# Performance work log

Measured on AMD Instinct MI355X. Metric: run time of the kernel, lower is better.

Reference implementation:

```python
import jax, jax.numpy as jnp
import numpy as np

N_OCTAVES = 32
N_SAMPLES = 32768
SAMPLERATE = 22050
MIN_HZ = 20
MAX_HZ = 3000
BASE_RESONANCE = 0.01


def setup_inputs() -> dict:
    key = jax.random.key(0)
    k1, k2, k3 = jax.random.split(key, 3)
    B, E = 4, 16
    return {
        "f0": jax.random.uniform(k1, (B, E, 1), dtype=jnp.float32),
        "decay_coefficients": jax.random.normal(k2, (B, E, 1), dtype=jnp.float32),
        "freq_spacing": jax.random.uniform(k3, (B, E, 1), dtype=jnp.float32),
    }


def reference(f0, decay_coefficients, freq_spacing):
    B, E, _ = f0.shape
    min_freq = MIN_HZ / (SAMPLERATE // 2)
    max_freq = MAX_HZ / (SAMPLERATE // 2)
    freq_range = max_freq - min_freq

    f0 = jnp.abs(f0)  # (B, E, 1)

    # exponential_decay: note the forward applies sigmoid BEFORE calling
    # exponential_decay, which applies sigmoid again -> double sigmoid.
    dv = jax.nn.sigmoid(jax.nn.sigmoid(decay_coefficients))  # (B, E, 1)
    resonance_factor = (1.0 - BASE_RESONANCE) * 0.99
    d = BASE_RESONANCE + dv * resonance_factor  # (B, E, 1)
    log_d = jnp.broadcast_to(jnp.log(d + 1e-12), (B, E, N_OCTAVES))
    # interpolate(size=n_frames) with in==out size is the identity, so skip it.
    exp_decays = jnp.exp(jnp.cumsum(log_d, axis=-1))  # (B, E, O)

    f0 = (min_freq + f0 * freq_range) * np.pi  # (B, E, 1)
    factors = jnp.cumsum(jnp.broadcast_to(freq_spacing, (B, E, N_OCTAVES)), axis=-1)
    f0s = f0 * factors  # (B, E, O)
    f0s = f0s * (f0s < 1).astype(f0s.dtype)  # mask partials above Nyquist

    # cumsum of a constant per-sample frequency == freq * (sample_index + 1)
    t = jnp.arange(1, N_SAMPLES + 1, dtype=f0s.dtype)  # (S,)
    phase = f0s[..., None] * t  # (B, E, O, S)
    osc = jnp.sin(phase) * exp_decays[..., None]  # (B, E, O, S)

    osc = jnp.sum(osc, axis=2)  # (B, E, S)
    mx = jnp.max(jnp.abs(osc), axis=-1, keepdims=True)
    return osc / (mx + 1e-8)
```

## Files before the change

kernel.cpp:

```cpp
#include <hip/hip_runtime.h>
#include <math.h>

#define N_OCT  32
#define N_SMP  32768
#define N_PAIR 64
#define BPP    32

__global__ __launch_bounds__(256) void f0res_osc(
    const float* __restrict__ f0_in,
    const float* __restrict__ dec_in,
    const float* __restrict__ fs_in,
    float* __restrict__ out,
    float* __restrict__ bmax)
{
    __shared__ __align__(16) float sw[N_OCT];
    __shared__ __align__(16) float sa[N_OCT];

    const int pair = blockIdx.x >> 5;
    const int blk  = blockIdx.x & (BPP - 1);
    const int tid  = threadIdx.x;

    if (tid < N_OCT) {
        const float minf   = (float)(20.0 / 11025.0);
        const float frange = (float)(3000.0 / 11025.0 - 20.0 / 11025.0);
        const float pif    = 3.14159265358979323846f;
        const float INV2PI = 0.15915494309189535f;

        float f0 = fabsf(f0_in[pair]);
        float fs = fs_in[pair];
        float x  = dec_in[pair];

        float s1 = 1.0f / (1.0f + expf(-x));
        float s2 = 1.0f / (1.0f + expf(-s1));
        float d  = 0.01f + s2 * (float)(0.99 * 0.99);
        float ld = logf(d + 1e-12f);
        float f0p = (minf + f0 * frange) * pif;

        float fac = 0.0f, acl = 0.0f, myfac = 0.0f, myacl = 0.0f;
#pragma unroll
        for (int o = 0; o < N_OCT; ++o) {
            fac += fs;
            acl += ld;
            if (o == tid) { myfac = fac; myacl = acl; }
        }
        float f0s = f0p * myfac;
        sw[tid] = (f0s < 1.0f) ? f0s * INV2PI : 0.0f;
        sa[tid] = expf(myacl);
    }
    __syncthreads();

    float4 wv[8], av[8];
    const float4* w4 = (const float4*)sw;
    const float4* a4 = (const float4*)sa;
#pragma unroll
    for (int i = 0; i < 8; ++i) { wv[i] = w4[i]; av[i] = a4[i]; }

    const int   s0 = (blk << 10) + tid;
    const float t0 = (float)(s0 + 1);
    const float t1 = (float)(s0 + 257);
    const float t2 = (float)(s0 + 513);
    const float t3 = (float)(s0 + 769);

    float acc0 = 0.0f, acc1 = 0.0f, acc2 = 0.0f, acc3 = 0.0f;
#pragma unroll
    for (int i = 0; i < 8; ++i) {
        const float wr[4] = { wv[i].x, wv[i].y, wv[i].z, wv[i].w };
        const float ar[4] = { av[i].x, av[i].y, av[i].z, av[i].w };
#pragma unroll
        for (int j = 0; j < 4; ++j) {
            float w = wr[j], a = ar[j];
            acc0 = fmaf(a, __builtin_amdgcn_sinf(__builtin_amdgcn_fractf(w * t0)), acc0);
            acc1 = fmaf(a, __builtin_amdgcn_sinf(__builtin_amdgcn_fractf(w * t1)), acc1);
            acc2 = fmaf(a, __builtin_amdgcn_sinf(__builtin_amdgcn_fractf(w * t2)), acc2);
            acc3 = fmaf(a, __builtin_amdgcn_sinf(__builtin_amdgcn_fractf(w * t3)), acc3);
        }
    }

    float* op = out + pair * N_SMP + s0;
    op[0]   = acc0;
    op[256] = acc1;
    op[512] = acc2;
    op[768] = acc3;

    float av_ = fmaxf(fmaxf(fabsf(acc0), fabsf(acc1)),
                      fmaxf(fabsf(acc2), fabsf(acc3)));
#pragma unroll
    for (int m = 32; m >= 1; m >>= 1)
        av_ = fmaxf(av_, __shfl_xor(av_, m, 64));
    __shared__ float wm[4];
    if ((tid & 63) == 0) wm[tid >> 6] = av_;
    __syncthreads();
    if (tid == 0)
        bmax[pair * BPP + blk] = fmaxf(fmaxf(wm[0], wm[1]), fmaxf(wm[2], wm[3]));
}

__global__ __launch_bounds__(256) void f0res_norm(
    float* __restrict__ out, const float* __restrict__ bmax)
{
    const int pair = blockIdx.x >> 5;
    const int tid  = threadIdx.x;

    float v = (tid < BPP) ? bmax[pair * BPP + tid] : 0.0f;
#pragma unroll
    for (int m = 16; m >= 1; m >>= 1)
        v = fmaxf(v, __shfl_xor(v, m, 64));
    v = __shfl(v, 0, 64);
    __shared__ float smx;
    if (tid == 0) smx = v;
    __syncthreads();
    const float inv = 1.0f / (smx + 1e-8f);

    const int idx = ((blockIdx.x & 31) << 8) + tid;
    float4* o4 = (float4*)(out + pair * N_SMP);
    float4 val = o4[idx];
    val.x *= inv; val.y *= inv; val.z *= inv; val.w *= inv;
    o4[idx] = val;
}

extern "C" void kernel_launch(void* const* d_in, const int* in_sizes, int n_in,
                              void* d_out, int out_size, void* d_ws, size_t ws_size,
                              hipStream_t stream) {
    const float* f0  = (const float*)d_in[0];
    const float* dec = (const float*)d_in[1];
    const float* fs  = (const float*)d_in[2];
    float* out = (float*)d_out;

    float* bmax = (float*)d_ws;

    f0res_osc <<<N_PAIR * BPP, 256, 0, stream>>>(f0, dec, fs, out, bmax);
    f0res_norm<<<N_PAIR * 32,  256, 0, stream>>>(out, bmax);
}
```

Baseline: 74.18 us.

## Replace per-sample sin with angle-addition recurrence across 8 strided samples

```diff
diff --git a/kernel.cpp b/kernel.cpp
--- a/kernel.cpp
+++ b/kernel.cpp
@@ -4,7 +4,9 @@
 #define N_OCT  32
 #define N_SMP  32768
 #define N_PAIR 64
-#define BPP    32
+#define BPP    16
+
+typedef float v2f __attribute__((ext_vector_type(2)));
 
 __global__ __launch_bounds__(256) void f0res_osc(
     const float* __restrict__ f0_in,
@@ -13,10 +15,9 @@
     float* __restrict__ out,
     float* __restrict__ bmax)
 {
-    __shared__ __align__(16) float sw[N_OCT];
-    __shared__ __align__(16) float sa[N_OCT];
+    __shared__ __align__(16) float4 sp[N_OCT];
 
-    const int pair = blockIdx.x >> 5;
+    const int pair = blockIdx.x >> 4;
     const int blk  = blockIdx.x & (BPP - 1);
     const int tid  = threadIdx.x;
 
@@ -44,46 +45,44 @@
             if (o == tid) { myfac = fac; myacl = acl; }
         }
         float f0s = f0p * myfac;
-        sw[tid] = (f0s < 1.0f) ? f0s * INV2PI : 0.0f;
-        sa[tid] = expf(myacl);
+        float w   = (f0s < 1.0f) ? f0s * INV2PI : 0.0f;
+        float dd  = __builtin_amdgcn_fractf(w * 256.0f);
+        sp[tid] = make_float4(w, expf(myacl),
+                              __builtin_amdgcn_cosf(dd),
+                              __builtin_amdgcn_sinf(dd));
     }
     __syncthreads();
 
-    float4 wv[8], av[8];
-    const float4* w4 = (const float4*)sw;
-    const float4* a4 = (const float4*)sa;
+    const int   s0 = (blk << 11) + tid;
+    const float t0 = (float)(s0 + 1);
+
+    float acc[8] = {0,0,0,0,0,0,0,0};
+    const float4* p4 = (const float4*)sp;
 #pragma unroll
-    for (int i = 0; i < 8; ++i) { wv[i] = w4[i]; av[i] = a4[i]; }
+    for (int o = 0; o < N_OCT; ++o) {
+        float4 prm = p4[o];
+        const float w = prm.x, a = prm.y;
+        const v2f C2 = { prm.z, prm.z };
+        const v2f S2 = { prm.w, prm.w };
 
-    const int   s0 = (blk << 10) + tid;
-    const float t0 = (float)(s0 + 1);
-    const float t1 = (float)(s0 + 257);
-    const float t2 = (float)(s0 + 513);
-    const float t3 = (float)(s0 + 769);
-
-    float acc0 = 0.0f, acc1 = 0.0f, acc2 = 0.0f, acc3 = 0.0f;
+        float r0 = __builtin_amdgcn_fractf(w * t0);
+        v2f sc = { __builtin_amdgcn_sinf(r0), __builtin_amdgcn_cosf(r0) };
+        acc[0] = fmaf(a, sc.x, acc[0]);
 #pragma unroll
-    for (int i = 0; i < 8; ++i) {
-        const float wr[4] = { wv[i].x, wv[i].y, wv[i].z, wv[i].w };
-        const float ar[4] = { av[i].x, av[i].y, av[i].z, av[i].w };
-#pragma unroll
-        for (int j = 0; j < 4; ++j) {
-            float w = wr[j], a = ar[j];
-            acc0 = fmaf(a, __builtin_amdgcn_sinf(__builtin_amdgcn_fractf(w * t0)), acc0);
-            acc1 = fmaf(a, __builtin_amdgcn_sinf(__builtin_amdgcn_fractf(w * t1)), acc1);
-            acc2 = fmaf(a, __builtin_amdgcn_sinf(__builtin_amdgcn_fractf(w * t2)), acc2);
-            acc3 = fmaf(a, __builtin_amdgcn_sinf(__builtin_amdgcn_fractf(w * t3)), acc3);
+        for (int k = 1; k < 8; ++k) {
+            v2f tmp = { sc.y, -sc.x };
+            sc = __builtin_elementwise_fma(sc, C2, tmp * S2);
+            acc[k] = fmaf(a, sc.x, acc[k]);
         }
     }
 
     float* op = out + pair * N_SMP + s0;
-    op[0]   = acc0;
-    op[256] = acc1;
-    op[512] = acc2;
-    op[768] = acc3;
+#pragma unroll
+    for (int k = 0; k < 8; ++k) op[k * 256] = acc[k];
 
-    float av_ = fmaxf(fmaxf(fabsf(acc0), fabsf(acc1)),
-                      fmaxf(fabsf(acc2), fabsf(acc3)));
+    float av_ = 0.0f;
+#pragma unroll
+    for (int k = 0; k < 8; ++k) av_ = fmaxf(av_, fabsf(acc[k]));
 #pragma unroll
     for (int m = 32; m >= 1; m >>= 1)
         av_ = fmaxf(av_, __shfl_xor(av_, m, 64));
@@ -102,9 +101,8 @@
 
     float v = (tid < BPP) ? bmax[pair * BPP + tid] : 0.0f;
 #pragma unroll
-    for (int m = 16; m >= 1; m >>= 1)
+    for (int m = 8; m >= 1; m >>= 1)
         v = fmaxf(v, __shfl_xor(v, m, 64));
-    v = __shfl(v, 0, 64);
     __shared__ float smx;
     if (tid == 0) smx = v;
     __syncthreads();
```

Measured after the change: 75.98 us. 1.02x slower.
